# Performance work log

Hardware: AMD Instinct MI355X
Metric: run time of the kernel (lower is better)

Reference implementation:

```python
import jax, jax.numpy as jnp
import numpy as np

B, F, H, P, L, A = 8192, 512, 1024, 64, 32, 16


def setup_inputs() -> dict:
    key = jax.random.key(0)
    ks = jax.random.split(key, 7)
    s = lambda k, shape, fan: jax.random.normal(k, shape, jnp.float32) / np.sqrt(fan)
    return {
        "state": jax.random.normal(ks[0], (B, F), jnp.float32),
        "W0": s(ks[1], (A, H, F), F),
        "b0": jnp.zeros((A, H), jnp.float32),
        "W1": s(ks[2], (A, H, H), H),
        "b1": jnp.zeros((A, H), jnp.float32),
        "W2": s(ks[3], (A, P, H), H),
        "ltl_corr": jax.random.normal(ks[4], (A, P), jnp.float32),
        # learned policies = {0..31}; active-only experts = policies 32..47
        "learned_idx": jnp.arange(L, dtype=jnp.int64),
        "active_idx": jnp.arange(L, L + A, dtype=jnp.int64),
    }


def reference(state, W0, b0, W1, b1, W2, ltl_corr, learned_idx, active_idx):
    # Batched over the A active experts (original loops in Python per expert).
    h = jax.nn.relu(jnp.einsum('bf,ahf->abh', state, W0) + b0[:, None, :])   # [A,B,H]
    h = jax.nn.relu(jnp.einsum('abh,agh->abg', h, W1) + b1[:, None, :])      # [A,B,H]
    x = jnp.einsum('abh,aph->abp', h, W2) + ltl_corr[:, None, :]             # [A,B,P]
    # softmax restricted to learned columns, scattered back into zeros
    sub = jax.nn.softmax(x[:, :, learned_idx], axis=-1)                       # [A,B,L]
    emb = jnp.zeros_like(x).at[:, :, learned_idx].set(sub)                    # [A,B,P]
    # all_emb starts as identity per batch element; active rows replaced
    all_emb = jnp.broadcast_to(jnp.eye(P, dtype=state.dtype), (state.shape[0], P, P))
    all_emb = all_emb.at[:, active_idx, :].set(jnp.transpose(emb, (1, 0, 2)))
    return all_emb
```

## Files before the change

### kernel.cpp

```cpp
#include <hip/hip_runtime.h>
#include <hip/hip_bf16.h>


typedef short v8s __attribute__((ext_vector_type(8)));
typedef float v4f __attribute__((ext_vector_type(4)));
using bf16 = __hip_bfloat16;

#define AS_GLOBAL __attribute__((address_space(1)))
#define AS_LDS    __attribute__((address_space(3)))

static constexpr int Mtot = 8192;
static constexpr int Fdim = 512;
static constexpr int Hdim = 1024;
static constexpr int Pdim = 64;
static constexpr int Aexp = 16;

__device__ __forceinline__ void gload_lds16(const void* g, void* l) {
  __builtin_amdgcn_global_load_lds((const AS_GLOBAL void*)g, (AS_LDS void*)l, 16, 0, 0);
}
__device__ __forceinline__ unsigned short bfu(float x) {
  bf16 h = __float2bfloat16(x);
  return *(unsigned short*)&h;
}
#define MFMA16(d, a, b) d = __builtin_amdgcn_mfma_f32_16x16x32_bf16(a, b, d, 0, 0, 0)
#define WAIT_VM3 asm volatile("s_waitcnt vmcnt(3)" ::: "memory")
#define WAIT_VM0 asm volatile("s_waitcnt vmcnt(0)" ::: "memory")
#define BAR() __builtin_amdgcn_s_barrier()

__device__ __forceinline__ void cvt_span(const float* __restrict__ src,
                                         unsigned short* __restrict__ dst, int n4,
                                         int gid, int nthr) {
  for (int i = gid; i < n4; i += nthr) {
    float4 v = ((const float4*)src)[i];
    ushort4 u;
    u.x = bfu(v.x); u.y = bfu(v.y); u.z = bfu(v.z); u.w = bfu(v.w);
    ((ushort4*)dst)[i] = u;
  }
}

__global__ void cvt_all_kernel(const float* __restrict__ s0, unsigned short* __restrict__ d0, int n0,
                               const float* __restrict__ s1, unsigned short* __restrict__ d1, int n1,
                               const float* __restrict__ s2, unsigned short* __restrict__ d2, int n2,
                               const float* __restrict__ s3, unsigned short* __restrict__ d3, int n3) {
  int gid = blockIdx.x * blockDim.x + threadIdx.x;
  int nthr = gridDim.x * blockDim.x;
  cvt_span(s0, d0, n0, gid, nthr);
  cvt_span(s1, d1, n1, gid, nthr);
  cvt_span(s2, d2, n2, gid, nthr);
  cvt_span(s3, d3, n3, gid, nthr);
}

__global__ void ident_kernel(float* __restrict__ outp) {
  const long total4 = (long)Mtot * Pdim * Pdim / 4;
  long i = blockIdx.x * 256 + threadIdx.x;
  const long stride = (long)gridDim.x * 256;
  for (; i < total4; i += stride) {
    long e = i * 4;
    int q = (int)(e & 63);
    int p = (int)((e >> 6) & 63);
    float4 v;
    v.x = (p == q) ? 1.f : 0.f;
    v.y = (p == q + 1) ? 1.f : 0.f;
    v.z = (p == q + 2) ? 1.f : 0.f;
    v.w = (p == q + 3) ? 1.f : 0.f;
    *(float4*)&outp[e] = v;
  }
}

template <int NT>
__global__ __launch_bounds__(256) void gemm97_kernel(
    const bf16* __restrict__ Ain, long aAmul,
    const bf16* __restrict__ Bw,
    const float* __restrict__ bias,
    bf16* __restrict__ Cout, long aCmul, int nbm) {
  constexpr int K = NT * 64;
  __shared__ short lsA[128 * 64];
  __shared__ short lsB[128 * 64];
  const int t = threadIdx.x;
  const int nwg = nbm * 128;

  const int flat = blockIdx.x;
  const int perx = nwg >> 3;
  const int swz = (flat & 7) * perx + (flat >> 3);
  const int perg = nbm * 8;
  const int g = swz / perg;
  const int e = swz % perg;
  const int msup = e >> 5;
  const int ny = (e >> 2) & 7;
  const int mloc = e & 3;
  const int mBase = (msup * 4 + mloc) * 128;
  const int nBase = ny * 128;

  const bf16* A0 = Ain + (size_t)g * aAmul;
  const bf16* B0 = Bw + (size_t)g * (1024 * K);
  const float* biasE = bias + g * 1024 + nBase;
  bf16* C0 = Cout + (size_t)g * aCmul + nBase;

  const int w = t >> 6, lane = t & 63;
  const int wm = w >> 1, wn = w & 1;
  const int lr = lane & 15, lk = lane >> 4;

  v4f acc[4][4];
#pragma unroll
  for (int m = 0; m < 4; ++m)
#pragma unroll
    for (int n = 0; n < 4; ++n) acc[m][n] = (v4f)(0.f);

  const int rowA = t >> 3;
  const int col8 = (t & 7) * 8;
  const bf16* gA = A0 + (size_t)(mBase + rowA) * K + col8;
  const bf16* gB = B0 + (size_t)(nBase + rowA) * K + col8;

  for (int k0 = 0; k0 < K; k0 += 64) {
#pragma unroll
    for (int i = 0; i < 4; ++i) {
      gload_lds16(gA + (size_t)(i * 32) * K + k0, &lsA[i * 2048 + t * 8]);
      gload_lds16(gB + (size_t)(i * 32) * K + k0, &lsB[i * 2048 + t * 8]);
    }
    __syncthreads();
#pragma unroll
    for (int kk = 0; kk < 2; ++kk) {
      v8s af[4], bfr[4];
#pragma unroll
      for (int m = 0; m < 4; ++m)
        af[m] = *(const v8s*)&lsA[(wm * 64 + m * 16 + lr) * 64 + kk * 32 + lk * 8];
#pragma unroll
      for (int n = 0; n < 4; ++n)
        bfr[n] = *(const v8s*)&lsB[(wn * 64 + n * 16 + lr) * 64 + kk * 32 + lk * 8];
#pragma unroll
      for (int m = 0; m < 4; ++m)
#pragma unroll
        for (int n = 0; n < 4; ++n)
          MFMA16(acc[m][n], af[m], bfr[n]);
    }
    __syncthreads();
  }

#pragma unroll
  for (int n = 0; n < 4; ++n) {
    const int colIn = wn * 64 + n * 16 + lr;
    const float bv = biasE[colIn];
#pragma unroll
    for (int m = 0; m < 4; ++m) {
      const int row0 = mBase + wm * 64 + m * 16 + lk * 4;
#pragma unroll
      for (int j = 0; j < 4; ++j) {
        float v = acc[m][n][j] + bv;
        v = v > 0.f ? v : 0.f;
        C0[(size_t)(row0 + j) * 1024 + colIn] = __float2bfloat16(v);
      }
    }
  }
}

__global__ __launch_bounds__(256) void gemm2_softmax_kernel(
    const bf16* __restrict__ h1, const bf16* __restrict__ W2b,
    const float* __restrict__ ltl, const int* __restrict__ lidx,
    const int* __restrict__ aidx, float* __restrict__ outp, int mGlobBase, int MC) {
  __shared__ short lsA[2][32 * 64];
  __shared__ short lsB[2][64 * 64];
  __shared__ float X[32][68];
  __shared__ int s_lidx[32];
  __shared__ int s_inv[64];
  __shared__ int s_arow;
  const int a = blockIdx.y;
  const bf16* Ain = h1 + (size_t)a * MC * Hdim;
  const bf16* Bw = W2b + (size_t)a * Pdim * Hdim;
  const float* ltlE = ltl + (size_t)a * Pdim;

  const int t = threadIdx.x;
  const int mBase = blockIdx.x * 32;
  const int w = t >> 6, lane = t & 63;
  const int lr = lane & 15, lk = lane >> 4;
  const int wr = w & 1, wq = w >> 1;

  if (t < 64) s_inv[t] = -1;
  __syncthreads();
  if (t < 32) {
    int q = lidx[t];
    s_lidx[t] = q;
    s_inv[q] = t;
  }
  if (t == 0) s_arow = aidx[a];
  __syncthreads();

  const int srow = t >> 3;
  const int sg = (t & 7) ^ ((t >> 3) & 7);
  const bf16* gA = Ain + (size_t)(mBase + srow) * Hdim + sg * 8;
  const bf16* gB = Bw + (size_t)srow * Hdim + sg * 8;

  auto stage = [&](int buf, int kt) {
    gload_lds16(gA + kt * 64, &lsA[buf][t * 8]);
    gload_lds16(gB + kt * 64, &lsB[buf][t * 8]);
    gload_lds16(gB + (size_t)32 * Hdim + kt * 64, &lsB[buf][2048 + t * 8]);
  };

  v4f acc[2];
  acc[0] = (v4f)(0.f); acc[1] = (v4f)(0.f);

  stage(0, 0);
  for (int kt = 0; kt < 16; ++kt) {
    const int buf = kt & 1;
    if (kt + 1 < 16) { stage(buf ^ 1, kt + 1); WAIT_VM3; } else { WAIT_VM0; }
    BAR();
#pragma unroll
    for (int s = 0; s < 2; ++s) {
      int rowA = wr * 16 + lr;
      v8s af = *(const v8s*)&lsA[buf][rowA * 64 + ((((s << 2) + lk) ^ (rowA & 7)) << 3)];
#pragma unroll
      for (int n = 0; n < 2; ++n) {
        int rowB = wq * 32 + n * 16 + lr;
        v8s bf = *(const v8s*)&lsB[buf][rowB * 64 + ((((s << 2) + lk) ^ (rowB & 7)) << 3)];
        MFMA16(acc[n], af, bf);
      }
    }
    BAR();
  }

#pragma unroll
  for (int n = 0; n < 2; ++n) {
    const int col = wq * 32 + n * 16 + lr;
    const float lc = ltlE[col];
#pragma unroll
    for (int j = 0; j < 4; ++j) {
      X[wr * 16 + lk * 4 + j][col] = acc[n][j] + lc;
    }
  }
  __syncthreads();

  if (t < 32) {
    const int r = t;
    float mx = -1e30f;
#pragma unroll
    for (int l = 0; l < 32; ++l) mx = fmaxf(mx, X[r][s_lidx[l]]);
    float s = 0.f;
#pragma unroll
    for (int l = 0; l < 32; ++l) s += __expf(X[r][s_lidx[l]] - mx);
    const float rs = 1.f / s;
    const size_t obase = ((size_t)(mGlobBase + mBase + r) * 64 + s_arow) * 64;
#pragma unroll
    for (int q0 = 0; q0 < 64; q0 += 4) {
      float4 v;
      v.x = (s_inv[q0 + 0] >= 0) ? __expf(X[r][q0 + 0] - mx) * rs : 0.f;
      v.y = (s_inv[q0 + 1] >= 0) ? __expf(X[r][q0 + 1] - mx) * rs : 0.f;
      v.z = (s_inv[q0 + 2] >= 0) ? __expf(X[r][q0 + 2] - mx) * rs : 0.f;
      v.w = (s_inv[q0 + 3] >= 0) ? __expf(X[r][q0 + 3] - mx) * rs : 0.f;
      *(float4*)&outp[obase + q0] = v;
    }
  }
}

extern "C" void kernel_launch(void* const* d_in, const int* in_sizes, int n_in,
                              void* d_out, int out_size, void* d_ws, size_t ws_size,
                              hipStream_t stream) {
  const float* state = (const float*)d_in[0];
  const float* W0 = (const float*)d_in[1];
  const float* b0 = (const float*)d_in[2];
  const float* W1 = (const float*)d_in[3];
  const float* b1 = (const float*)d_in[4];
  const float* W2 = (const float*)d_in[5];
  const float* ltl = (const float*)d_in[6];
  const int* lidx = (const int*)d_in[7];
  const int* aidx = (const int*)d_in[8];
  float* outp = (float*)d_out;

  char* ws = (char*)d_ws;
  bf16* stateb = (bf16*)ws;
  bf16* W0b = stateb + (size_t)Mtot * Fdim;
  bf16* W1b = W0b + (size_t)Aexp * Hdim * Fdim;
  bf16* W2b = W1b + (size_t)Aexp * Hdim * Hdim;
  bf16* h0 = W2b + (size_t)Aexp * Pdim * Hdim;
  const size_t fixedB = (size_t)(Mtot * Fdim + Aexp * Hdim * Fdim +
                                 Aexp * Hdim * Hdim + Aexp * Pdim * Hdim) * 2;
  int MC = 2048;
  while (MC > 512 && fixedB + (size_t)2 * Aexp * MC * Hdim * 2 + 4096 > ws_size) MC >>= 1;
  bf16* h1 = h0 + (size_t)Aexp * MC * Hdim;

  ident_kernel<<<dim3(4096), dim3(256), 0, stream>>>(outp);
  cvt_all_kernel<<<dim3(2048), dim3(256), 0, stream>>>(
      state, (unsigned short*)stateb, Mtot * Fdim / 4,
      W0, (unsigned short*)W0b, Aexp * Hdim * Fdim / 4,
      W1, (unsigned short*)W1b, Aexp * Hdim * Hdim / 4,
      W2, (unsigned short*)W2b, Aexp * Pdim * Hdim / 4);

  const int nbm = MC / 128;
  for (int mOff = 0; mOff < Mtot; mOff += MC) {
    gemm97_kernel<Fdim / 64><<<dim3(nbm * 128), dim3(256), 0, stream>>>(
        stateb + (size_t)mOff * Fdim, 0L,
        W0b, b0, h0, (long)MC * Hdim, nbm);
    gemm97_kernel<Hdim / 64><<<dim3(nbm * 128), dim3(256), 0, stream>>>(
        h0, (long)MC * Hdim,
        W1b, b1, h1, (long)MC * Hdim, nbm);
    gemm2_softmax_kernel<<<dim3(MC / 32, Aexp), dim3(256), 0, stream>>>(
        h1, W2b, ltl, lidx, aidx, outp, mOff, MC);
  }
}
```

Baseline: 756.2 us.

## Replace 128x128 GEMM with double-buffered 256x256 tile kernel using swizzled LDS

Replaces the first two expert GEMMs with a 512-thread kernel that computes 256x256 output tiles. LDS is double-buffered, so the next K-slice is loaded by direct global-to-LDS copies while MFMAs run on the current slice. The work is split into four quadrant phases with barriers, partial vmcnt waits and raised wave priority around the MFMA blocks, and LDS rows are XOR-swizzled to avoid bank conflicts. This targets the old kernel's serialized load-then-compute loop and its lower data reuse. In exchange it uses far more LDS and registers per block, which lowers occupancy, and the hand-tuned wait counts are fragile.

```diff
diff --git a/kernel.cpp b/kernel.cpp
--- a/kernel.cpp
+++ b/kernel.cpp
@@ -23,8 +23,11 @@
   return *(unsigned short*)&h;
 }
 #define MFMA16(d, a, b) d = __builtin_amdgcn_mfma_f32_16x16x32_bf16(a, b, d, 0, 0, 0)
+#define WAIT_VM4 asm volatile("s_waitcnt vmcnt(4)" ::: "memory")
 #define WAIT_VM3 asm volatile("s_waitcnt vmcnt(3)" ::: "memory")
+#define WAIT_VM2 asm volatile("s_waitcnt vmcnt(2)" ::: "memory")
 #define WAIT_VM0 asm volatile("s_waitcnt vmcnt(0)" ::: "memory")
+#define WAIT_LGKM0 asm volatile("s_waitcnt lgkmcnt(0)" ::: "memory")
 #define BAR() __builtin_amdgcn_s_barrier()
 
 __device__ __forceinline__ void cvt_span(const float* __restrict__ src,
@@ -68,84 +71,155 @@
 }
 
 template <int NT>
-__global__ __launch_bounds__(256) void gemm97_kernel(
+__global__ __launch_bounds__(512, 2) void gemm256_kernel(
     const bf16* __restrict__ Ain, long aAmul,
     const bf16* __restrict__ Bw,
     const float* __restrict__ bias,
     bf16* __restrict__ Cout, long aCmul, int nbm) {
   constexpr int K = NT * 64;
-  __shared__ short lsA[128 * 64];
-  __shared__ short lsB[128 * 64];
+  __shared__ short sA[2][256 * 64];
+  __shared__ short sB[2][256 * 64];
   const int t = threadIdx.x;
-  const int nwg = nbm * 128;
-
+  const int nwg = nbm * 4 * Aexp;
   const int flat = blockIdx.x;
   const int perx = nwg >> 3;
   const int swz = (flat & 7) * perx + (flat >> 3);
-  const int perg = nbm * 8;
+  const int perg = nbm * 4;
   const int g = swz / perg;
   const int e = swz % perg;
-  const int msup = e >> 5;
-  const int ny = (e >> 2) & 7;
-  const int mloc = e & 3;
-  const int mBase = (msup * 4 + mloc) * 128;
-  const int nBase = ny * 128;
+  const int mt = e >> 2;
+  const int nt = e & 3;
+  const int mBase = mt * 256, nBase = nt * 256;
 
   const bf16* A0 = Ain + (size_t)g * aAmul;
   const bf16* B0 = Bw + (size_t)g * (1024 * K);
   const float* biasE = bias + g * 1024 + nBase;
-  bf16* C0 = Cout + (size_t)g * aCmul + nBase;
+  bf16* C0 = Cout + (size_t)g * aCmul;
 
   const int w = t >> 6, lane = t & 63;
-  const int wm = w >> 1, wn = w & 1;
+  const int wm = w & 1, wn = w >> 1;
   const int lr = lane & 15, lk = lane >> 4;
 
-  v4f acc[4][4];
-#pragma unroll
-  for (int m = 0; m < 4; ++m)
+  const int srow = t >> 3;
+  const int sg = (t & 7) ^ (srow & 7);
+  const bf16* gA = A0 + (size_t)(mBase + srow) * K + sg * 8;
+  const bf16* gB = B0 + (size_t)(nBase + srow) * K + sg * 8;
+  auto stA = [&](int bufi, int half, int i, int kt) {
+    gload_lds16(gA + (size_t)(half * 128 + i * 64) * K + kt * 64,
+                &sA[bufi][(half * 128 + i * 64) * 64 + t * 8]);
+  };
+  auto stB = [&](int bufi, int half, int i, int kt) {
+    gload_lds16(gB + (size_t)(half * 128 + i * 64) * K + kt * 64,
+                &sB[bufi][(half * 128 + i * 64) * 64 + t * 8]);
+  };
+
+  v4f acc[8][4];
+#pragma unroll
+  for (int m = 0; m < 8; ++m)
 #pragma unroll
     for (int n = 0; n < 4; ++n) acc[m][n] = (v4f)(0.f);
 
-  const int rowA = t >> 3;
-  const int col8 = (t & 7) * 8;
-  const bf16* gA = A0 + (size_t)(mBase + rowA) * K + col8;
-  const bf16* gB = B0 + (size_t)(nBase + rowA) * K + col8;
-
-  for (int k0 = 0; k0 < K; k0 += 64) {
-#pragma unroll
-    for (int i = 0; i < 4; ++i) {
-      gload_lds16(gA + (size_t)(i * 32) * K + k0, &lsA[i * 2048 + t * 8]);
-      gload_lds16(gB + (size_t)(i * 32) * K + k0, &lsB[i * 2048 + t * 8]);
-    }
-    __syncthreads();
-#pragma unroll
-    for (int kk = 0; kk < 2; ++kk) {
-      v8s af[4], bfr[4];
-#pragma unroll
-      for (int m = 0; m < 4; ++m)
-        af[m] = *(const v8s*)&lsA[(wm * 64 + m * 16 + lr) * 64 + kk * 32 + lk * 8];
-#pragma unroll
-      for (int n = 0; n < 4; ++n)
-        bfr[n] = *(const v8s*)&lsB[(wn * 64 + n * 16 + lr) * 64 + kk * 32 + lk * 8];
-#pragma unroll
-      for (int m = 0; m < 4; ++m)
-#pragma unroll
-        for (int n = 0; n < 4; ++n)
-          MFMA16(acc[m][n], af[m], bfr[n]);
-    }
-    __syncthreads();
-  }
-
-#pragma unroll
-  for (int n = 0; n < 4; ++n) {
-    const int colIn = wn * 64 + n * 16 + lr;
-    const float bv = biasE[colIn];
-#pragma unroll
-    for (int m = 0; m < 4; ++m) {
-      const int row0 = mBase + wm * 64 + m * 16 + lk * 4;
+  v8s a[4][2], b[2][2];
+  const int xg = lr & 7;
+
+  stA(0, 0, 0, 0); stA(0, 0, 1, 0);
+  stB(0, 0, 0, 0); stB(0, 0, 1, 0);
+  stB(0, 1, 0, 0); stB(0, 1, 1, 0);
+  stA(0, 1, 0, 0); stA(0, 1, 1, 0);
+  WAIT_VM0;
+  BAR();
+
+  for (int kt = 0; kt < NT; ++kt) {
+    const int cur = kt & 1, nb = cur ^ 1;
+    const bool pf = (kt + 1) < NT;
+    const short* cA = sA[cur];
+    const short* cB = sB[cur];
+
+    auto rdA = [&](int mh) {
+#pragma unroll
+      for (int mf = 0; mf < 4; ++mf)
+#pragma unroll
+        for (int ks = 0; ks < 2; ++ks) {
+          const int row = (mh * 4 + mf) * 32 + wm * 16 + lr;
+          a[mf][ks] = *(const v8s*)&cA[row * 64 + (((ks * 4 + lk) ^ xg) << 3)];
+        }
+    };
+    auto rdB = [&](int nh) {
+#pragma unroll
+      for (int nf = 0; nf < 2; ++nf)
+#pragma unroll
+        for (int ks = 0; ks < 2; ++ks) {
+          const int row = (nh * 2 + nf) * 64 + wn * 16 + lr;
+          b[nf][ks] = *(const v8s*)&cB[row * 64 + (((ks * 4 + lk) ^ xg) << 3)];
+        }
+    };
+
+    rdA(0); rdB(0);
+    if (pf) { stA(nb, 0, 0, kt + 1); stA(nb, 0, 1, kt + 1); }
+    BAR(); WAIT_LGKM0;
+    __builtin_amdgcn_s_setprio(1);
+#pragma unroll
+    for (int ks = 0; ks < 2; ++ks)
+#pragma unroll
+      for (int mf = 0; mf < 4; ++mf)
+#pragma unroll
+        for (int nf = 0; nf < 2; ++nf) MFMA16(acc[mf][nf], a[mf][ks], b[nf][ks]);
+    __builtin_amdgcn_s_setprio(0);
+    if (pf) { WAIT_VM4; } else { WAIT_VM2; }
+    BAR();
+
+    rdB(1);
+    if (pf) { stB(nb, 0, 0, kt + 1); stB(nb, 0, 1, kt + 1); }
+    BAR(); WAIT_LGKM0;
+    __builtin_amdgcn_s_setprio(1);
+#pragma unroll
+    for (int ks = 0; ks < 2; ++ks)
+#pragma unroll
+      for (int mf = 0; mf < 4; ++mf)
+#pragma unroll
+        for (int nf = 0; nf < 2; ++nf) MFMA16(acc[mf][2 + nf], a[mf][ks], b[nf][ks]);
+    __builtin_amdgcn_s_setprio(0);
+    if (pf) { WAIT_VM4; } else { WAIT_VM0; }
+    BAR();
+
+    rdA(1); rdB(0);
+    if (pf) { stB(nb, 1, 0, kt + 1); stB(nb, 1, 1, kt + 1); }
+    BAR(); WAIT_LGKM0;
+    __builtin_amdgcn_s_setprio(1);
+#pragma unroll
+    for (int ks = 0; ks < 2; ++ks)
+#pragma unroll
+      for (int mf = 0; mf < 4; ++mf)
+#pragma unroll
+        for (int nf = 0; nf < 2; ++nf) MFMA16(acc[4 + mf][nf], a[mf][ks], b[nf][ks]);
+    __builtin_amdgcn_s_setprio(0);
+    BAR();
+
+    rdB(1);
+    if (pf) { stA(nb, 1, 0, kt + 1); stA(nb, 1, 1, kt + 1); }
+    BAR(); WAIT_LGKM0;
+    __builtin_amdgcn_s_setprio(1);
+#pragma unroll
+    for (int ks = 0; ks < 2; ++ks)
+#pragma unroll
+      for (int mf = 0; mf < 4; ++mf)
+#pragma unroll
+        for (int nf = 0; nf < 2; ++nf) MFMA16(acc[4 + mf][2 + nf], a[mf][ks], b[nf][ks]);
+    __builtin_amdgcn_s_setprio(0);
+    if (pf) { WAIT_VM4; }
+    BAR();
+  }
+
+#pragma unroll
+  for (int nf = 0; nf < 4; ++nf) {
+    const int colIn = nBase + nf * 64 + wn * 16 + lr;
+    const float bv = biasE[nf * 64 + wn * 16 + lr];
+#pragma unroll
+    for (int mf = 0; mf < 8; ++mf) {
+      const int row0 = mBase + mf * 32 + wm * 16 + lk * 4;
 #pragma unroll
       for (int j = 0; j < 4; ++j) {
-        float v = acc[m][n][j] + bv;
+        float v = acc[mf][nf][j] + bv;
         v = v > 0.f ? v : 0.f;
         C0[(size_t)(row0 + j) * 1024 + colIn] = __float2bfloat16(v);
       }
@@ -283,12 +357,12 @@
       W1, (unsigned short*)W1b, Aexp * Hdim * Hdim / 4,
       W2, (unsigned short*)W2b, Aexp * Pdim * Hdim / 4);
 
-  const int nbm = MC / 128;
+  const int nbm = MC / 256;
   for (int mOff = 0; mOff < Mtot; mOff += MC) {
-    gemm97_kernel<Fdim / 64><<<dim3(nbm * 128), dim3(256), 0, stream>>>(
+    gemm256_kernel<Fdim / 64><<<dim3(nbm * 4 * Aexp), dim3(512), 0, stream>>>(
         stateb + (size_t)mOff * Fdim, 0L,
         W0b, b0, h0, (long)MC * Hdim, nbm);
-    gemm97_kernel<Hdim / 64><<<dim3(nbm * 128), dim3(256), 0, stream>>>(
+    gemm256_kernel<Hdim / 64><<<dim3(nbm * 4 * Aexp), dim3(512), 0, stream>>>(
         h0, (long)MC * Hdim,
         W1b, b1, h1, (long)MC * Hdim, nbm);
     gemm2_softmax_kernel<<<dim3(MC / 32, Aexp), dim3(256), 0, stream>>>(
```

Result: faster. 623.9 us (-17.5%).
